# Optimization experiments

Measured on AMD Instinct MI355X. Metric: run time of the kernel, lower is better.

Reference implementation:

```python
import jax, jax.numpy as jnp
import numpy as np

EMBED = 1024
HEADS = 16
HEAD_DIM = EMBED // HEADS


def setup_inputs() -> dict:
    key = jax.random.key(0)
    ks = jax.random.split(key, 11)
    B, S = 4, 2048
    scale = 0.02
    inp = {
        "value": jax.random.normal(ks[0], (B, S, EMBED), jnp.float32),
        "key": jax.random.normal(ks[1], (B, S, EMBED), jnp.float32),
        "query": jax.random.normal(ks[2], (B, S, EMBED), jnp.float32),
        "Wv": jax.random.normal(ks[3], (EMBED, EMBED), jnp.float32) * scale,
        "bv": jax.random.normal(ks[4], (EMBED,), jnp.float32) * scale,
        "Wk": jax.random.normal(ks[5], (EMBED, EMBED), jnp.float32) * scale,
        "bk": jax.random.normal(ks[6], (EMBED,), jnp.float32) * scale,
        "Wq": jax.random.normal(ks[7], (EMBED, EMBED), jnp.float32) * scale,
        "bq": jax.random.normal(ks[8], (EMBED,), jnp.float32) * scale,
        "Wo": jax.random.normal(ks[9], (EMBED, EMBED), jnp.float32) * scale,
        "bo": jax.random.normal(ks[10], (EMBED,), jnp.float32) * scale,
    }
    return inp


def reference(value, key, query, Wv, bv, Wk, bk, Wq, bq, Wo, bo):
    B, Sq, E = query.shape
    # linear projections (torch Linear: x @ W.T + b; here W stored as [in, out])
    v = (value @ Wv + bv).reshape(B, -1, HEADS, HEAD_DIM)   # [B,Skv,H,D]
    k = (key @ Wk + bk).reshape(B, -1, HEADS, HEAD_DIM)
    q = (query @ Wq + bq).reshape(B, Sq, HEADS, HEAD_DIM)
    # scaled dot-product attention, full score matrix [B,H,Sq,Skv]
    energy = jnp.einsum("bqhd,bkhd->bhqk", q, k) / jnp.sqrt(jnp.float32(HEAD_DIM))
    attn = jax.nn.softmax(energy, axis=-1)
    out = jnp.einsum("bhqk,bkhd->bqhd", attn, v).reshape(B, Sq, E)
    return out @ Wo + bo
```

## Files before the change

kernel.cpp:

```cpp
#include <hip/hip_runtime.h>
#include <hip/hip_bf16.h>
#include <stdint.h>

typedef unsigned short u16;
typedef __bf16 bf16_t;
typedef bf16_t bf16x8 __attribute__((ext_vector_type(8)));
typedef float f32x4 __attribute__((ext_vector_type(4)));

__device__ __forceinline__ u16 f2b(float f) {
    union { float f; uint32_t i; } v; v.f = f;
    uint32_t r = v.i + 0x7FFFu + ((v.i >> 16) & 1u);
    return (u16)(r >> 16);
}
__device__ __forceinline__ uint32_t pk2(float a, float b) {
    __hip_bfloat162 h = __float22bfloat162_rn(float2{a, b});
    return *(const uint32_t*)&h;
}
__device__ __forceinline__ uint4 pack8(float4 lo, float4 hi) {
    uint4 r;
    r.x = pk2(lo.x, lo.y); r.y = pk2(lo.z, lo.w);
    r.z = pk2(hi.x, hi.y); r.w = pk2(hi.z, hi.w);
    return r;
}
__device__ __forceinline__ void async16(const u16* g, u16* l) {
    __builtin_amdgcn_global_load_lds(
        (const __attribute__((address_space(1))) uint32_t*)g,
        (__attribute__((address_space(3))) uint32_t*)l,
        16, 0, 0);
}

template<bool XF32>
__device__ __forceinline__ void gemm128(const void* __restrict__ Xv,
                                        const u16* __restrict__ WT,
                                        const float* __restrict__ bias,
                                        u16* __restrict__ dstb,
                                        float* __restrict__ dstf, int mode,
                                        int m0, int n0)
{
    __shared__ __align__(16) u16 As[128 * 64];
    __shared__ __align__(16) u16 Bs[128 * 64];
    const int t    = threadIdx.x;
    const int lane = t & 63;
    const int quad = lane >> 4;
    const int l15  = lane & 15;
    const int wave = t >> 6;
    const int wm = (wave >> 1) * 64;
    const int wn = (wave & 1) * 64;

    f32x4 acc[4][4];
#pragma unroll
    for (int i = 0; i < 4; i++)
#pragma unroll
        for (int j = 0; j < 4; j++)
#pragma unroll
            for (int r = 0; r < 4; r++) acc[i][j][r] = 0.0f;

    int rr[4], lb[4];
#pragma unroll
    for (int c = 0; c < 4; c++) {
        const int ci = c * 256 + t;
        rr[c] = ci >> 3;
        lb[c] = (ci & 7) ^ (rr[c] & 7);
    }

    for (int kt = 0; kt < 1024; kt += 64) {
        __syncthreads();
#pragma unroll
        for (int c = 0; c < 4; c++)
            async16(WT + (n0 + rr[c]) * 1024 + kt + lb[c] * 8, &Bs[(c * 256 + t) * 8]);
        if (XF32) {
#pragma unroll
            for (int c = 0; c < 4; c++) {
                const float* g = (const float*)Xv + (m0 + rr[c]) * 1024 + kt + lb[c] * 8;
                const float4 lo = *(const float4*)g;
                const float4 hi = *(const float4*)(g + 4);
                *(uint4*)&As[(c * 256 + t) * 8] = pack8(lo, hi);
            }
        } else {
#pragma unroll
            for (int c = 0; c < 4; c++)
                async16((const u16*)Xv + (m0 + rr[c]) * 1024 + kt + lb[c] * 8,
                        &As[(c * 256 + t) * 8]);
        }
        __syncthreads();

#pragma unroll
        for (int kk = 0; kk < 64; kk += 32) {
            bf16x8 af[4], bfv[4];
#pragma unroll
            for (int i = 0; i < 4; i++) {
                const int ra = wm + i * 16 + l15;
                const int rb2 = wn + i * 16 + l15;
                af[i]  = *(const bf16x8*)&As[ra * 64 + (((kk >> 3) + quad) ^ (l15 & 7)) * 8];
                bfv[i] = *(const bf16x8*)&Bs[rb2 * 64 + (((kk >> 3) + quad) ^ (l15 & 7)) * 8];
            }
#pragma unroll
            for (int i = 0; i < 4; i++)
#pragma unroll
                for (int j = 0; j < 4; j++)
                    acc[i][j] = __builtin_amdgcn_mfma_f32_16x16x32_bf16(af[i], bfv[j], acc[i][j], 0, 0, 0);
        }
    }

#pragma unroll
    for (int i = 0; i < 4; i++) {
        const int rb = m0 + wm + i * 16 + quad * 4;
#pragma unroll
        for (int j = 0; j < 4; j++) {
            const int col = n0 + wn + j * 16 + l15;
            const float bias_v = bias[col];
            if (mode == 2) {
                const int b = rb >> 11, s = rb & 2047;
                const int h = col >> 6, d = col & 63;
                uint2 pk;
                pk.x = pk2(acc[i][j][0] + bias_v, acc[i][j][1] + bias_v);
                pk.y = pk2(acc[i][j][2] + bias_v, acc[i][j][3] + bias_v);
                *(uint2*)&dstb[((b * 16 + h) * 64 + d) * 2048 + s] = pk;
            } else {
#pragma unroll
                for (int r = 0; r < 4; r++) {
                    const float v = acc[i][j][r] + bias_v;
                    const int gm = rb + r;
                    if (mode == 0) {
                        const int b = gm >> 11, s = gm & 2047;
                        const int h = col >> 6, d = col & 63;
                        dstb[((b * 16 + h) * 2048 + s) * 64 + d] = f2b(v);
                    } else {
                        dstf[gm * 1024 + col] = v;
                    }
                }
            }
        }
    }
}

__global__ __launch_bounds__(256)
void convert_x(const float* __restrict__ q_in, const float* __restrict__ k_in,
               const float* __restrict__ v_in, u16* __restrict__ Xb)
{
    const int z = blockIdx.y;
    const float* src = (z == 0) ? q_in : (z == 1) ? k_in : v_in;
    u16* dst = Xb + z * (8 * 1024 * 1024);
    const int i = (blockIdx.x * 256 + threadIdx.x) * 8;
    const float4 lo = *(const float4*)(src + i);
    const float4 hi = *(const float4*)(src + i + 4);
    *(uint4*)(dst + i) = pack8(lo, hi);
}

__global__ __launch_bounds__(256)
void qkv_kernel_f32(const float* __restrict__ q_in, const float* __restrict__ k_in,
                    const float* __restrict__ v_in, const u16* __restrict__ WT,
                    const float* __restrict__ bq, const float* __restrict__ bk,
                    const float* __restrict__ bv,
                    u16* __restrict__ Qo, u16* __restrict__ Ko, u16* __restrict__ VTo)
{
    const int z = blockIdx.z;
    const float* X   = (z == 0) ? q_in : (z == 1) ? k_in : v_in;
    const u16* wt    = WT + ((z == 0) ? 2 : (z == 1) ? 1 : 0) * (1024 * 1024);
    const float* bias= (z == 0) ? bq : (z == 1) ? bk : bv;
    u16* dst         = (z == 0) ? Qo : (z == 1) ? Ko : VTo;
    gemm128<true>(X, wt, bias, dst, nullptr, (z == 2) ? 2 : 0,
                  blockIdx.y * 128, blockIdx.x * 128);
}

__global__ __launch_bounds__(256)
void qkv_kernel_b16(const u16* __restrict__ Xb, const u16* __restrict__ WT,
                    const float* __restrict__ bq, const float* __restrict__ bk,
                    const float* __restrict__ bv,
                    u16* __restrict__ Qo, u16* __restrict__ Ko, u16* __restrict__ VTo)
{
    const int z = blockIdx.z;
    const u16* X     = Xb + z * (8 * 1024 * 1024);
    const u16* wt    = WT + ((z == 0) ? 2 : (z == 1) ? 1 : 0) * (1024 * 1024);
    const float* bias= (z == 0) ? bq : (z == 1) ? bk : bv;
    u16* dst         = (z == 0) ? Qo : (z == 1) ? Ko : VTo;
    const int s = blockIdx.y * 8 + blockIdx.x;
    const int o = (s & 7) * 64 + (s >> 3);
    gemm128<false>(X, wt, bias, dst, nullptr, (z == 2) ? 2 : 0,
                   (o >> 3) * 128, (o & 7) * 128);
}

__global__ __launch_bounds__(256)
void oproj_kernel(const u16* __restrict__ AO, const u16* __restrict__ WT,
                  const float* __restrict__ bo, float* __restrict__ out)
{
    const int s = blockIdx.y * 8 + blockIdx.x;
    const int o = (s & 7) * 64 + (s >> 3);
    gemm128<false>(AO, WT + 3 * 1024 * 1024, bo, nullptr, out, 1,
                   (o >> 3) * 128, (o & 7) * 128);
}

__global__ void transpose_w(const float* __restrict__ Wv, const float* __restrict__ Wk,
                            const float* __restrict__ Wq, const float* __restrict__ Wo,
                            u16* __restrict__ WT)
{
    __shared__ u16 tile[64][65];
    const int z = blockIdx.z;
    const float* W = (z == 0) ? Wv : (z == 1) ? Wk : (z == 2) ? Wq : Wo;
    u16* dst = WT + z * 1024 * 1024;
    const int r0 = blockIdx.y * 64, c0 = blockIdx.x * 64;
    const int col = threadIdx.x & 63, rb = threadIdx.x >> 6;
#pragma unroll
    for (int r = rb; r < 64; r += 4) tile[r][col] = f2b(W[(r0 + r) * 1024 + c0 + col]);
    __syncthreads();
#pragma unroll
    for (int r = rb; r < 64; r += 4) dst[(c0 + r) * 1024 + r0 + col] = tile[col][r];
}

__global__ __launch_bounds__(256, 3)
void attn_kernel(const u16* __restrict__ Q, const u16* __restrict__ K,
                 const u16* __restrict__ VT, u16* __restrict__ AO)
{
    __shared__ __align__(16) u16 Ks[128 * 64];
    __shared__ __align__(16) u16 Ps[64 * 128];
    __shared__ __align__(16) u16 Vts[80 * 128];

    const int t    = threadIdx.x;
    const int lane = t & 63;
    const int wave = t >> 6;
    const int quad = lane >> 4;
    const int l15  = lane & 15;
    const int bh = blockIdx.y;
    const int qt = blockIdx.x;

    const u16* Qg = Q + (bh * 2048 + qt * 64) * 64;
    const u16* Kg = K + bh * 2048 * 64;
    const u16* Vg = VT + bh * 64 * 2048;

    const u16* kgp[4];
    const u16* vgp[4];
    u16* kld[4];
    u16* vld[4];
#pragma unroll
    for (int c = 0; c < 4; c++) {
        const int ci = c * 256 + t;
        const int krr = ci >> 3, klb = (ci & 7)  ^ (krr & 7);
        const int vrr = ci >> 4, vlb = (ci & 15) ^ (vrr & 15);
        kgp[c] = Kg + krr * 64 + klb * 8;
        vgp[c] = Vg + vrr * 2048 + vlb * 8;
        kld[c] = &Ks[ci * 8];
        vld[c] = &Vts[ci * 8];
    }

#pragma unroll
    for (int c = 0; c < 4; c++) {
        async16(kgp[c], kld[c]);
        kgp[c] += 128 * 64;
    }

    {
        const int idx = t * 8;
        const int row = 64 + (idx >> 7);
        const u16 one = 0x3F80;
        u16 vals[8];
#pragma unroll
        for (int i = 0; i < 8; i++) vals[i] = (row == 64) ? one : (u16)0;
        *(uint4*)&Vts[64 * 128 + idx] = *(uint4*)vals;
    }

    bf16x8 bqr[2];
    {
        const u16* qrow = Qg + (wave * 16 + l15) * 64 + quad * 8;
#pragma unroll
        for (int c = 0; c < 2; c++) {
            uint4 dv = *(const uint4*)(qrow + c * 32);
            u16 tmp[8];
            *(uint4*)tmp = dv;
            float f[8];
#pragma unroll
            for (int i = 0; i < 8; i++) {
                union { float f; uint32_t u; } x; x.u = ((uint32_t)tmp[i]) << 16;
                f[i] = x.f * 0.18033688f;
            }
            uint4 pk;
            pk.x = pk2(f[0], f[1]); pk.y = pk2(f[2], f[3]);
            pk.z = pk2(f[4], f[5]); pk.w = pk2(f[6], f[7]);
            bqr[c] = *(bf16x8*)&pk;
        }
    }

    f32x4 o[5];
#pragma unroll
    for (int dj = 0; dj < 5; dj++)
#pragma unroll
        for (int r = 0; r < 4; r++) o[dj][r] = 0.0f;
    float m_st = 0.0f;
    f32x4 cinit;
#pragma unroll
    for (int r = 0; r < 4; r++) cinit[r] = 0.0f;

    int ak_off[2][8];
#pragma unroll
    for (int ki = 0; ki < 2; ki++)
#pragma unroll
        for (int n = 0; n < 8; n++)
            ak_off[ki][n] = (n * 16 + l15) * 64 + (((ki * 4) + quad) ^ (l15 & 7)) * 8;
    int av_off[4][5], bp_off[4], pw_off[8];
#pragma unroll
    for (int ks = 0; ks < 4; ks++) {
        bp_off[ks] = (wave * 16 + l15) * 128 + ((ks * 4 + quad) ^ l15) * 8;
#pragma unroll
        for (int dj = 0; dj < 5; dj++)
            av_off[ks][dj] = (dj * 16 + l15) * 128 + ((ks * 4 + quad) ^ l15) * 8;
    }
#pragma unroll
    for (int n = 0; n < 8; n++)
        pw_off[n] = (wave * 16 + l15) * 128 + ((2 * n + (quad >> 1)) ^ l15) * 8
                    + (quad & 1) * 4;

    for (int kv = 0; kv < 16; kv++) {
        __syncthreads();
#pragma unroll
        for (int c = 0; c < 4; c++) {
            async16(vgp[c], vld[c]);
            vgp[c] += 128;
        }

        f32x4 s[8];
#pragma unroll
        for (int n = 0; n < 8; n++)
            s[n] = __builtin_amdgcn_mfma_f32_16x16x32_bf16(
                *(const bf16x8*)&Ks[ak_off[0][n]], bqr[0], cinit, 0, 0, 0);
#pragma unroll
        for (int n = 0; n < 8; n++)
            s[n] = __builtin_amdgcn_mfma_f32_16x16x32_bf16(
                *(const bf16x8*)&Ks[ak_off[1][n]], bqr[1], s[n], 0, 0, 0);

        __syncthreads();
        if (kv < 15) {
#pragma unroll
            for (int c = 0; c < 4; c++) {
                async16(kgp[c], kld[c]);
                kgp[c] += 128 * 64;
            }
        }

        float mxn[8];
#pragma unroll
        for (int n = 0; n < 8; n++)
            mxn[n] = fmaxf(fmaxf(s[n][0], s[n][1]), fmaxf(s[n][2], s[n][3]));
        float mx = fmaxf(fmaxf(fmaxf(mxn[0], mxn[1]), fmaxf(mxn[2], mxn[3])),
                         fmaxf(fmaxf(mxn[4], mxn[5]), fmaxf(mxn[6], mxn[7])));
        if (__any(mx > 8.0f)) {
            mx = fmaxf(mx, __shfl_xor(mx, 16));
            mx = fmaxf(mx, __shfl_xor(mx, 32));
            const float dm = fmaxf(mx, 0.0f);
            const float alpha = exp2f(-dm);
#pragma unroll
            for (int n = 0; n < 8; n++)
#pragma unroll
                for (int r = 0; r < 4; r++) s[n][r] -= dm;
            m_st += dm;
#pragma unroll
            for (int r = 0; r < 4; r++) cinit[r] = -m_st;
#pragma unroll
            for (int dj = 0; dj < 5; dj++)
#pragma unroll
                for (int r = 0; r < 4; r++) o[dj][r] *= alpha;
        }

#pragma unroll
        for (int n = 0; n < 8; n++) {
            uint2 pk;
            pk.x = pk2(exp2f(s[n][0]), exp2f(s[n][1]));
            pk.y = pk2(exp2f(s[n][2]), exp2f(s[n][3]));
            *(uint2*)&Ps[pw_off[n]] = pk;
        }
        asm volatile("s_waitcnt lgkmcnt(0)" ::: "memory");

#pragma unroll
        for (int ks = 0; ks < 4; ks++) {
            const bf16x8 bp = *(const bf16x8*)&Ps[bp_off[ks]];
#pragma unroll
            for (int dj = 0; dj < 5; dj++) {
                const bf16x8 av = *(const bf16x8*)&Vts[av_off[ks][dj]];
                o[dj] = __builtin_amdgcn_mfma_f32_16x16x32_bf16(av, bp, o[dj], 0, 0, 0);
            }
        }
    }

    const float lsum = __shfl(o[4][0], l15);
    const int b = bh >> 4, h = bh & 15;
    const int sq = qt * 64 + wave * 16 + l15;
    const float inv = 1.0f / lsum;
#pragma unroll
    for (int dj = 0; dj < 4; dj++) {
        uint2 pk;
        pk.x = pk2(o[dj][0] * inv, o[dj][1] * inv);
        pk.y = pk2(o[dj][2] * inv, o[dj][3] * inv);
        *(uint2*)&AO[(b * 2048 + sq) * 1024 + h * 64 + dj * 16 + quad * 4] = pk;
    }
}

extern "C" void kernel_launch(void* const* d_in, const int* in_sizes, int n_in,
                              void* d_out, int out_size, void* d_ws, size_t ws_size,
                              hipStream_t stream)
{
    (void)in_sizes; (void)n_in; (void)out_size;
    const float* value = (const float*)d_in[0];
    const float* key_  = (const float*)d_in[1];
    const float* query = (const float*)d_in[2];
    const float* Wv = (const float*)d_in[3];
    const float* bv = (const float*)d_in[4];
    const float* Wk = (const float*)d_in[5];
    const float* bk = (const float*)d_in[6];
    const float* Wq = (const float*)d_in[7];
    const float* bq = (const float*)d_in[8];
    const float* Wo = (const float*)d_in[9];
    const float* bo = (const float*)d_in[10];

    u16* ws = (u16*)d_ws;
    u16* WT = ws;
    u16* Q  = ws + 4 * 1024 * 1024;
    u16* K  = Q + 8 * 1024 * 1024;
    u16* VT = K + 8 * 1024 * 1024;
    u16* AO = VT + 8 * 1024 * 1024;
    u16* Xb = AO + 8 * 1024 * 1024;
    const size_t need = (size_t)(4 + 8 + 8 + 8 + 8 + 24) * 1024 * 1024 * sizeof(u16);

    transpose_w<<<dim3(16, 16, 4), dim3(256), 0, stream>>>(Wv, Wk, Wq, Wo, WT);
    if (ws_size >= need) {
        convert_x<<<dim3(4096, 3), dim3(256), 0, stream>>>(query, key_, value, Xb);
        qkv_kernel_b16<<<dim3(8, 64, 3), dim3(256), 0, stream>>>(Xb, WT, bq, bk, bv,
                                                                 Q, K, VT);
    } else {
        qkv_kernel_f32<<<dim3(8, 64, 3), dim3(256), 0, stream>>>(query, key_, value,
                                                                 WT, bq, bk, bv,
                                                                 Q, K, VT);
    }
    attn_kernel<<<dim3(32, 64), dim3(256), 0, stream>>>(Q, K, VT, AO);
    oproj_kernel<<<dim3(8, 64, 1), dim3(256), 0, stream>>>(AO, WT, bo, (float*)d_out);
}
```

Baseline: 380.2 us.

## Double-buffer GEMM tiles and hold the attention ones-row in registers

New measurement: 360.6 us. 5.2% less time.

```diff
diff --git a/kernel.cpp b/kernel.cpp
--- a/kernel.cpp
+++ b/kernel.cpp
@@ -37,8 +37,8 @@
                                         float* __restrict__ dstf, int mode,
                                         int m0, int n0)
 {
-    __shared__ __align__(16) u16 As[128 * 64];
-    __shared__ __align__(16) u16 Bs[128 * 64];
+    __shared__ __align__(16) u16 As[2][128 * 64];
+    __shared__ __align__(16) u16 Bs[2][128 * 64];
     const int t    = threadIdx.x;
     const int lane = t & 63;
     const int quad = lane >> 4;
@@ -63,26 +63,36 @@
         lb[c] = (ci & 7) ^ (rr[c] & 7);
     }
 
+#define STAGE_TILE(buf, kt)                                                         \
+    do {                                                                            \
+        _Pragma("unroll")                                                           \
+        for (int c = 0; c < 4; c++)                                                 \
+            async16(WT + (n0 + rr[c]) * 1024 + (kt) + lb[c] * 8,                    \
+                    &Bs[buf][(c * 256 + t) * 8]);                                   \
+        if (XF32) {                                                                 \
+            _Pragma("unroll")                                                       \
+            for (int c = 0; c < 4; c++) {                                           \
+                const float* g = (const float*)Xv + (m0 + rr[c]) * 1024 + (kt)      \
+                                 + lb[c] * 8;                                       \
+                const float4 lo = *(const float4*)g;                                \
+                const float4 hi = *(const float4*)(g + 4);                          \
+                *(uint4*)&As[buf][(c * 256 + t) * 8] = pack8(lo, hi);               \
+            }                                                                       \
+        } else {                                                                    \
+            _Pragma("unroll")                                                       \
+            for (int c = 0; c < 4; c++)                                             \
+                async16((const u16*)Xv + (m0 + rr[c]) * 1024 + (kt) + lb[c] * 8,    \
+                        &As[buf][(c * 256 + t) * 8]);                               \
+        }                                                                           \
+    } while (0)
+
+    STAGE_TILE(0, 0);
+    __syncthreads();
+
+    int cur = 0;
     for (int kt = 0; kt < 1024; kt += 64) {
-        __syncthreads();
-#pragma unroll
-        for (int c = 0; c < 4; c++)
-            async16(WT + (n0 + rr[c]) * 1024 + kt + lb[c] * 8, &Bs[(c * 256 + t) * 8]);
-        if (XF32) {
-#pragma unroll
-            for (int c = 0; c < 4; c++) {
-                const float* g = (const float*)Xv + (m0 + rr[c]) * 1024 + kt + lb[c] * 8;
-                const float4 lo = *(const float4*)g;
-                const float4 hi = *(const float4*)(g + 4);
-                *(uint4*)&As[(c * 256 + t) * 8] = pack8(lo, hi);
-            }
-        } else {
-#pragma unroll
-            for (int c = 0; c < 4; c++)
-                async16((const u16*)Xv + (m0 + rr[c]) * 1024 + kt + lb[c] * 8,
-                        &As[(c * 256 + t) * 8]);
-        }
-        __syncthreads();
+        if (kt < 960)
+            STAGE_TILE(cur ^ 1, kt + 64);
 
 #pragma unroll
         for (int kk = 0; kk < 64; kk += 32) {
@@ -91,8 +101,8 @@
             for (int i = 0; i < 4; i++) {
                 const int ra = wm + i * 16 + l15;
                 const int rb2 = wn + i * 16 + l15;
-                af[i]  = *(const bf16x8*)&As[ra * 64 + (((kk >> 3) + quad) ^ (l15 & 7)) * 8];
-                bfv[i] = *(const bf16x8*)&Bs[rb2 * 64 + (((kk >> 3) + quad) ^ (l15 & 7)) * 8];
+                af[i]  = *(const bf16x8*)&As[cur][ra * 64 + (((kk >> 3) + quad) ^ (l15 & 7)) * 8];
+                bfv[i] = *(const bf16x8*)&Bs[cur][rb2 * 64 + (((kk >> 3) + quad) ^ (l15 & 7)) * 8];
             }
 #pragma unroll
             for (int i = 0; i < 4; i++)
@@ -100,7 +110,11 @@
                 for (int j = 0; j < 4; j++)
                     acc[i][j] = __builtin_amdgcn_mfma_f32_16x16x32_bf16(af[i], bfv[j], acc[i][j], 0, 0, 0);
         }
-    }
+
+        __syncthreads();
+        cur ^= 1;
+    }
+#undef STAGE_TILE
 
 #pragma unroll
     for (int i = 0; i < 4; i++) {
@@ -213,7 +227,7 @@
 {
     __shared__ __align__(16) u16 Ks[128 * 64];
     __shared__ __align__(16) u16 Ps[64 * 128];
-    __shared__ __align__(16) u16 Vts[80 * 128];
+    __shared__ __align__(16) u16 Vts[64 * 128];
 
     const int t    = threadIdx.x;
     const int lane = t & 63;
@@ -248,14 +262,13 @@
         kgp[c] += 128 * 64;
     }
 
+    bf16x8 aones;
     {
-        const int idx = t * 8;
-        const int row = 64 + (idx >> 7);
-        const u16 one = 0x3F80;
+        const u16 one = (l15 == 0) ? (u16)0x3F80 : (u16)0;
         u16 vals[8];
 #pragma unroll
-        for (int i = 0; i < 8; i++) vals[i] = (row == 64) ? one : (u16)0;
-        *(uint4*)&Vts[64 * 128 + idx] = *(uint4*)vals;
+        for (int i = 0; i < 8; i++) vals[i] = one;
+        aones = *(bf16x8*)vals;
     }
 
     bf16x8 bqr[2];
@@ -295,12 +308,12 @@
 #pragma unroll
         for (int n = 0; n < 8; n++)
             ak_off[ki][n] = (n * 16 + l15) * 64 + (((ki * 4) + quad) ^ (l15 & 7)) * 8;
-    int av_off[4][5], bp_off[4], pw_off[8];
+    int av_off[4][4], bp_off[4], pw_off[8];
 #pragma unroll
     for (int ks = 0; ks < 4; ks++) {
         bp_off[ks] = (wave * 16 + l15) * 128 + ((ks * 4 + quad) ^ l15) * 8;
 #pragma unroll
-        for (int dj = 0; dj < 5; dj++)
+        for (int dj = 0; dj < 4; dj++)
             av_off[ks][dj] = (dj * 16 + l15) * 128 + ((ks * 4 + quad) ^ l15) * 8;
     }
 #pragma unroll
@@ -372,10 +385,11 @@
         for (int ks = 0; ks < 4; ks++) {
             const bf16x8 bp = *(const bf16x8*)&Ps[bp_off[ks]];
 #pragma unroll
-            for (int dj = 0; dj < 5; dj++) {
+            for (int dj = 0; dj < 4; dj++) {
                 const bf16x8 av = *(const bf16x8*)&Vts[av_off[ks][dj]];
                 o[dj] = __builtin_amdgcn_mfma_f32_16x16x32_bf16(av, bp, o[dj], 0, 0, 0);
             }
+            o[4] = __builtin_amdgcn_mfma_f32_16x16x32_bf16(aones, bp, o[4], 0, 0, 0);
         }
     }
 
```
